# Optimization experiments

Hardware: AMD Instinct MI355X
Metric: run time of the kernel (lower is better)

The kernel has to match this reference:

```python
import jax, jax.numpy as jnp
import numpy as np

K, N = 1024, 16384


def setup_inputs() -> dict:
    key = jax.random.key(0)
    k0, k1, k2 = jax.random.split(key, 3)
    # event counts (non-negative), like the COVID case-count observations
    obs = jax.random.uniform(k0, (K, N), dtype=jnp.float32) * 10.0
    # Beta ~ U(1, 3), Alpha ~ U(0, 0.01) per the torch parameter init
    Beta = 1.0 + 2.0 * jax.random.uniform(k1, (K,), dtype=jnp.float32)
    Alpha = 0.01 * jax.random.uniform(k2, (K, K), dtype=jnp.float32)
    return {"obs": obs, "Beta": Beta, "Alpha": Alpha}


def reference(obs, Beta, Alpha):
    """Hawkes log-likelihood, exact O(N*K) recursion replacing the O(N^2*K^2) loop.

    Original per-step math (t > 0):
      lam1[k, t] = softplus( sum_j Alpha[k, j] * sum_{tp < t} obs[j, tp] * Beta[j] * exp(-(t - tp) * Beta[j]) )
    The exponential kernel gives S_{t+1} = exp(-Beta) * (S_t + obs[:, t]), S_0 = 0,
    where S_t[j] = sum_{tp < t} obs[j, tp] * exp(-(t - tp) * Beta[j]).
    lam1[:, 0] = 0 exactly (the torch code returns zeros at t = 0, not softplus(0)).
    """
    Mu0 = obs.mean(axis=1) / 10.0 + 1e-5                      # [K] background rate
    decay = jnp.exp(-Beta)                                    # [K]

    def step(S, o_t):                                         # S: [K], o_t: [K]
        return decay * (S + o_t), S                           # emit S_t, carry S_{t+1}

    _, S_seq = jax.lax.scan(step, jnp.zeros_like(Beta), obs.T)  # S_seq: [N, K]

    G = Beta[None, :] * S_seq                                 # [N, K] = Beta_j * S_t[j]
    lam1 = jax.nn.softplus(G @ Alpha.T).T                     # [K, N]; row k = softplus(Alpha @ g_t)
    lam1 = lam1.at[:, 0].set(0.0)                             # t = 0 branch returns zeros

    lams0 = jnp.broadcast_to(Mu0[:, None], obs.shape)         # [K, N]
    Nloglams = obs * jnp.log(lams0 + lam1 + 1e-5)
    loglik = (Nloglams - lams0 - lam1).sum()
    return loglik, lams0, lam1
```

## Files before the change

kernel.cpp:

```cpp
#include <hip/hip_runtime.h>
#include <hip/hip_bf16.h>
#include <stdint.h>

#define K_DIM 1024
#define N_DIM 16384

typedef __attribute__((ext_vector_type(8))) short short8;
typedef __attribute__((ext_vector_type(4))) float floatx4;

__device__ __forceinline__ void async_copy16(const void* g, void* l) {
  __builtin_amdgcn_global_load_lds((const __attribute__((address_space(1))) void*)g,
                                   (__attribute__((address_space(3))) void*)l,
                                   16, 0, 0);
}

__device__ __forceinline__ unsigned short f2bf(float x) {
  uint32_t u = __float_as_uint(x);
  u += 0x7fffu + ((u >> 16) & 1u);
  return (unsigned short)(u >> 16);
}

__global__ __launch_bounds__(256) void convert_alpha(const float* __restrict__ A,
                                                     unsigned short* __restrict__ Abf) {
  int idx = (blockIdx.x * 256 + threadIdx.x) * 4;
  floatx4 v = *(const floatx4*)(A + idx);
  ushort4 o;
  o.x = f2bf(v[0]); o.y = f2bf(v[1]); o.z = f2bf(v[2]); o.w = f2bf(v[3]);
  *(ushort4*)(Abf + idx) = o;
}

__global__ __launch_bounds__(256) void mu_kernel(const float* __restrict__ obs,
                                                 float* __restrict__ mu_acc) {
  const int k = blockIdx.x;
  const float* row = obs + (size_t)k * N_DIM;
  float s = 0.f;
  for (int t = threadIdx.x * 4; t < N_DIM; t += 256 * 4) {
    float4 v = *(const float4*)(row + t);
    s += (v.x + v.y) + (v.z + v.w);
  }
  #pragma unroll
  for (int off = 32; off > 0; off >>= 1) s += __shfl_down(s, off);
  __shared__ float ws[4];
  if ((threadIdx.x & 63) == 0) ws[threadIdx.x >> 6] = s;
  __syncthreads();
  if (threadIdx.x == 0) mu_acc[k] = (ws[0] + ws[1]) + (ws[2] + ws[3]);
}

__global__ __launch_bounds__(256) void scan_kernel(const float* __restrict__ obs,
                                                   const float* __restrict__ Beta,
                                                   unsigned short* __restrict__ Gt) {
  __shared__ float tile[64][161];
  const int tw = blockIdx.x;
  const int jg = blockIdx.y;
  const int j0 = jg * 64;
  const int t0 = tw * 128;
  const int tid = threadIdx.x;

  for (int u = tid; u < 64 * 40; u += 256) {
    int row = u / 40;
    int c4 = u % 40;
    int tloc = c4 * 4;
    int tg = t0 - 32 + tloc;
    float4 v;
    if (tg >= 0) {
      v = *(const float4*)(obs + (size_t)(j0 + row) * N_DIM + tg);
    } else {
      v = make_float4(0.f, 0.f, 0.f, 0.f);
    }
    tile[row][tloc]     = v.x;
    tile[row][tloc + 1] = v.y;
    tile[row][tloc + 2] = v.z;
    tile[row][tloc + 3] = v.w;
  }
  __syncthreads();

  const int w = tid >> 6;
  const int lane = tid & 63;
  const int j = j0 + lane;
  const float beta = Beta[j];
  const float decay = expf(-beta);
  const int lt0 = w * 32;
  float S = 0.f;
  #pragma unroll
  for (int i = 0; i < 32; ++i) S = decay * (S + tile[lane][lt0 + i]);
  const int tg = t0 + w * 32;
  #pragma unroll
  for (int i = 0; i < 32; ++i) {
    Gt[(size_t)(tg + i) * K_DIM + j] = f2bf(beta * S);
    S = decay * (S + tile[lane][lt0 + 32 + i]);
  }
}

__global__ __launch_bounds__(256) void gemm_kernel(const unsigned short* __restrict__ A,
                                                   const unsigned short* __restrict__ B,
                                                   const float* __restrict__ obs,
                                                   const float* __restrict__ mu_acc,
                                                   float* __restrict__ lam1_out,
                                                   double* __restrict__ acc_out) {
  const int tb = blockIdx.x;
  const int kb = blockIdx.y;
  const int tid = threadIdx.x;
  const int lane = tid & 63, w = tid >> 6;
  const int wm = w >> 1, wn = w & 1;
  const int ml = lane & 15, q = lane >> 4;

  __shared__ unsigned short As[128 * 64];
  __shared__ unsigned short Bs[128 * 64];
  __shared__ float wsum[4];

  floatx4 acc[4][4] = {};

  const unsigned short* Ab = A + (size_t)kb * 128 * K_DIM;
  const unsigned short* Bb = B + (size_t)tb * 128 * K_DIM;

  for (int kt = 0; kt < 16; ++kt) {
    const unsigned short* Ak = Ab + kt * 64;
    const unsigned short* Bk = Bb + kt * 64;
    #pragma unroll
    for (int it = 0; it < 4; ++it) {
      int L = w * 256 + it * 64 + lane;
      int r = L >> 3;
      int c = L & 7;
      int cg = c ^ (r & 7);
      async_copy16(Ak + (size_t)r * K_DIM + cg * 8, &As[L * 8]);
      async_copy16(Bk + (size_t)r * K_DIM + cg * 8, &Bs[L * 8]);
    }
    __syncthreads();

    #pragma unroll
    for (int kk = 0; kk < 2; ++kk) {
      short8 a[4], b[4];
      #pragma unroll
      for (int mf = 0; mf < 4; ++mf) {
        int r = wm * 64 + mf * 16 + ml;
        int c = (kk * 4 + q) ^ (r & 7);
        a[mf] = *(const short8*)&As[r * 64 + c * 8];
      }
      #pragma unroll
      for (int nf = 0; nf < 4; ++nf) {
        int r = wn * 64 + nf * 16 + ml;
        int c = (kk * 4 + q) ^ (r & 7);
        b[nf] = *(const short8*)&Bs[r * 64 + c * 8];
      }
      #pragma unroll
      for (int mf = 0; mf < 4; ++mf)
        #pragma unroll
        for (int nf = 0; nf < 4; ++nf)
          acc[mf][nf] = __builtin_amdgcn_mfma_f32_16x16x32_bf16(a[mf], b[nf], acc[mf][nf], 0, 0, 0);
    }
    __syncthreads();
  }

  float lsum = 0.f;
  const int kblk = kb * 128 + wm * 64;
  const int tblk = tb * 128 + wn * 64;
  #pragma unroll
  for (int mf = 0; mf < 4; ++mf) {
    int k4 = kblk + mf * 16 + q * 4;
    floatx4 mu4 = *(const floatx4*)&mu_acc[k4];
    #pragma unroll
    for (int r = 0; r < 4; ++r) {
      int k = k4 + r;
      float mu = mu4[r] * (1.0f / 163840.0f) + 1e-5f;
      #pragma unroll
      for (int nf = 0; nf < 4; ++nf) {
        int t = tblk + nf * 16 + ml;
        float raw = acc[mf][nf][r];
        float e = __expf(-fabsf(raw));
        float lam = fmaxf(raw, 0.f) + __logf(1.f + e);
        if (t == 0) lam = 0.f;
        lam1_out[(size_t)k * N_DIM + t] = lam;
        float o = obs[(size_t)k * N_DIM + t];
        lsum += o * __logf(mu + lam + 1e-5f) - mu - lam;
      }
    }
  }
  #pragma unroll
  for (int off = 32; off > 0; off >>= 1) lsum += __shfl_down(lsum, off);
  if (lane == 0) wsum[w] = lsum;
  __syncthreads();
  if (tid == 0) atomicAdd(acc_out, (double)(wsum[0] + wsum[1] + wsum[2] + wsum[3]));
}

__global__ __launch_bounds__(256) void finalize_kernel(const float* __restrict__ mu_acc,
                                                       const double* __restrict__ acc,
                                                       float* __restrict__ out) {
  int k = blockIdx.x;
  float mu = mu_acc[k] * (1.0f / 163840.0f) + 1e-5f;
  float* dst = out + 1 + (size_t)k * N_DIM;
  int tid = threadIdx.x;
  if (tid < 3) dst[tid] = mu;
  float4 v4 = make_float4(mu, mu, mu, mu);
  for (int t = 3 + tid * 4; t + 3 < N_DIM; t += 256 * 4) *(float4*)(dst + t) = v4;
  if (tid == 3) dst[N_DIM - 1] = mu;
  if (blockIdx.x == 0 && tid == 4) out[0] = (float)(*acc);
}

extern "C" void kernel_launch(void* const* d_in, const int* in_sizes, int n_in,
                              void* d_out, int out_size, void* d_ws, size_t ws_size,
                              hipStream_t stream) {
  const float* obs   = (const float*)d_in[0];
  const float* Beta  = (const float*)d_in[1];
  const float* Alpha = (const float*)d_in[2];
  float* out = (float*)d_out;

  double* acc   = (double*)d_ws;
  float* mu_acc = (float*)((char*)d_ws + 16);

  unsigned short* Gt  = (unsigned short*)(out + 4);
  unsigned short* Abf = Gt + (size_t)N_DIM * K_DIM;

  hipMemsetAsync(d_ws, 0, 16, stream);

  convert_alpha<<<dim3(K_DIM * K_DIM / (256 * 4)), 256, 0, stream>>>(Alpha, Abf);

  mu_kernel<<<dim3(K_DIM), 256, 0, stream>>>(obs, mu_acc);

  scan_kernel<<<dim3(N_DIM / 128, K_DIM / 64), 256, 0, stream>>>(obs, Beta, Gt);

  gemm_kernel<<<dim3(N_DIM / 128, K_DIM / 128), 256, 0, stream>>>(
      Abf, Gt, obs, mu_acc, out + 1 + (size_t)K_DIM * N_DIM, acc);

  finalize_kernel<<<dim3(K_DIM), 256, 0, stream>>>(mu_acc, acc, out);
}
```

Measured before the change: 294.7 us.

## Switch GEMM to scaled FP8 inputs and fuse lams0 writes and Alpha conversion

Alpha and the scan output G are quantized to scaled e4m3 FP8, and the GEMM uses fp8 MFMA with an inverse scale applied in the epilogue. This halves the G intermediate traffic and the LDS footprint and uses the faster FP8 matrix path. The Alpha conversion is fused into the mu kernel. When the workspace is large enough, the intermediates live in the workspace, the lams0 broadcast is written in the GEMM epilogue, and the finalize pass is replaced by a one-thread tail kernel. FP8 quantization of Alpha and G adds precision risk to lam1 and to the log-likelihood.

New measurement: 287.3 us. -2.5%, faster.

```diff
diff --git a/kernel.cpp b/kernel.cpp
--- a/kernel.cpp
+++ b/kernel.cpp
@@ -5,7 +5,6 @@
 #define K_DIM 1024
 #define N_DIM 16384
 
-typedef __attribute__((ext_vector_type(8))) short short8;
 typedef __attribute__((ext_vector_type(4))) float floatx4;
 
 __device__ __forceinline__ void async_copy16(const void* g, void* l) {
@@ -14,41 +13,40 @@
                                    16, 0, 0);
 }
 
-__device__ __forceinline__ unsigned short f2bf(float x) {
-  uint32_t u = __float_as_uint(x);
-  u += 0x7fffu + ((u >> 16) & 1u);
-  return (unsigned short)(u >> 16);
-}
-
-__global__ __launch_bounds__(256) void convert_alpha(const float* __restrict__ A,
-                                                     unsigned short* __restrict__ Abf) {
-  int idx = (blockIdx.x * 256 + threadIdx.x) * 4;
-  floatx4 v = *(const floatx4*)(A + idx);
-  ushort4 o;
-  o.x = f2bf(v[0]); o.y = f2bf(v[1]); o.z = f2bf(v[2]); o.w = f2bf(v[3]);
-  *(ushort4*)(Abf + idx) = o;
-}
-
-__global__ __launch_bounds__(256) void mu_kernel(const float* __restrict__ obs,
-                                                 float* __restrict__ mu_acc) {
+__device__ __forceinline__ int pk4_e4m3(float a, float b, float c, float d) {
+  int lo = __builtin_amdgcn_cvt_pk_fp8_f32(a, b, 0, false);
+  return __builtin_amdgcn_cvt_pk_fp8_f32(c, d, lo, true);
+}
+
+#define A_SCALE 512.0f
+#define G_SCALE 32.0f
+#define INV_SCALE (1.0f / (512.0f * 32.0f))
+
+__global__ __launch_bounds__(256) void mu_convert(const float* __restrict__ obs,
+                                                  const float* __restrict__ Alpha,
+                                                  float* __restrict__ mu_acc,
+                                                  int* __restrict__ A8) {
   const int k = blockIdx.x;
+  const int tid = threadIdx.x;
   const float* row = obs + (size_t)k * N_DIM;
   float s = 0.f;
-  for (int t = threadIdx.x * 4; t < N_DIM; t += 256 * 4) {
+  for (int t = tid * 4; t < N_DIM; t += 256 * 4) {
     float4 v = *(const float4*)(row + t);
     s += (v.x + v.y) + (v.z + v.w);
   }
   #pragma unroll
   for (int off = 32; off > 0; off >>= 1) s += __shfl_down(s, off);
   __shared__ float ws[4];
-  if ((threadIdx.x & 63) == 0) ws[threadIdx.x >> 6] = s;
+  if ((tid & 63) == 0) ws[tid >> 6] = s;
+  float4 av = *(const float4*)(Alpha + (size_t)k * K_DIM + tid * 4);
+  A8[k * 256 + tid] = pk4_e4m3(av.x * A_SCALE, av.y * A_SCALE, av.z * A_SCALE, av.w * A_SCALE);
   __syncthreads();
-  if (threadIdx.x == 0) mu_acc[k] = (ws[0] + ws[1]) + (ws[2] + ws[3]);
+  if (tid == 0) mu_acc[k] = (ws[0] + ws[1]) + (ws[2] + ws[3]);
 }
 
 __global__ __launch_bounds__(256) void scan_kernel(const float* __restrict__ obs,
                                                    const float* __restrict__ Beta,
-                                                   unsigned short* __restrict__ Gt) {
+                                                   unsigned char* __restrict__ Gt8) {
   __shared__ float tile[64][161];
   const int tw = blockIdx.x;
   const int jg = blockIdx.y;
@@ -78,7 +76,7 @@
   const int lane = tid & 63;
   const int j = j0 + lane;
   const float beta = Beta[j];
-  const float decay = expf(-beta);
+  const float decay = __expf(-beta);
   const int lt0 = w * 32;
   float S = 0.f;
   #pragma unroll
@@ -86,16 +84,18 @@
   const int tg = t0 + w * 32;
   #pragma unroll
   for (int i = 0; i < 32; ++i) {
-    Gt[(size_t)(tg + i) * K_DIM + j] = f2bf(beta * S);
+    int p = __builtin_amdgcn_cvt_pk_fp8_f32(G_SCALE * beta * S, 0.f, 0, false);
+    Gt8[(size_t)(tg + i) * K_DIM + j] = (unsigned char)(p & 0xff);
     S = decay * (S + tile[lane][lt0 + 32 + i]);
   }
 }
 
-__global__ __launch_bounds__(256) void gemm_kernel(const unsigned short* __restrict__ A,
-                                                   const unsigned short* __restrict__ B,
+__global__ __launch_bounds__(256) void gemm_kernel(const unsigned char* __restrict__ A8,
+                                                   const unsigned char* __restrict__ B8,
                                                    const float* __restrict__ obs,
                                                    const float* __restrict__ mu_acc,
                                                    float* __restrict__ lam1_out,
+                                                   float* __restrict__ lams0_out,
                                                    double* __restrict__ acc_out) {
   const int tb = blockIdx.x;
   const int kb = blockIdx.y;
@@ -104,49 +104,51 @@
   const int wm = w >> 1, wn = w & 1;
   const int ml = lane & 15, q = lane >> 4;
 
-  __shared__ unsigned short As[128 * 64];
-  __shared__ unsigned short Bs[128 * 64];
+  __shared__ unsigned char As[128 * 64];
+  __shared__ unsigned char Bs[128 * 64];
   __shared__ float wsum[4];
 
   floatx4 acc[4][4] = {};
 
-  const unsigned short* Ab = A + (size_t)kb * 128 * K_DIM;
-  const unsigned short* Bb = B + (size_t)tb * 128 * K_DIM;
+  const unsigned char* Ab = A8 + (size_t)kb * 128 * K_DIM;
+  const unsigned char* Bb = B8 + (size_t)tb * 128 * K_DIM;
 
   for (int kt = 0; kt < 16; ++kt) {
-    const unsigned short* Ak = Ab + kt * 64;
-    const unsigned short* Bk = Bb + kt * 64;
+    const unsigned char* Ak = Ab + kt * 64;
+    const unsigned char* Bk = Bb + kt * 64;
     #pragma unroll
-    for (int it = 0; it < 4; ++it) {
-      int L = w * 256 + it * 64 + lane;
-      int r = L >> 3;
-      int c = L & 7;
-      int cg = c ^ (r & 7);
-      async_copy16(Ak + (size_t)r * K_DIM + cg * 8, &As[L * 8]);
-      async_copy16(Bk + (size_t)r * K_DIM + cg * 8, &Bs[L * 8]);
+    for (int it = 0; it < 2; ++it) {
+      int L = it * 256 + tid;
+      int r = L >> 2;
+      int c = L & 3;
+      int cg = c ^ ((r >> 1) & 3);
+      async_copy16(Ak + (size_t)r * K_DIM + cg * 16, &As[L * 16]);
+      async_copy16(Bk + (size_t)r * K_DIM + cg * 16, &Bs[L * 16]);
     }
     __syncthreads();
 
     #pragma unroll
     for (int kk = 0; kk < 2; ++kk) {
-      short8 a[4], b[4];
+      long a[4], b[4];
+      const int c0 = kk * 2 + (q >> 1);
+      const int sub = (q & 1) * 8;
       #pragma unroll
       for (int mf = 0; mf < 4; ++mf) {
         int r = wm * 64 + mf * 16 + ml;
-        int c = (kk * 4 + q) ^ (r & 7);
-        a[mf] = *(const short8*)&As[r * 64 + c * 8];
+        int cg = c0 ^ ((r >> 1) & 3);
+        a[mf] = *(const long*)&As[r * 64 + cg * 16 + sub];
       }
       #pragma unroll
       for (int nf = 0; nf < 4; ++nf) {
         int r = wn * 64 + nf * 16 + ml;
-        int c = (kk * 4 + q) ^ (r & 7);
-        b[nf] = *(const short8*)&Bs[r * 64 + c * 8];
+        int cg = c0 ^ ((r >> 1) & 3);
+        b[nf] = *(const long*)&Bs[r * 64 + cg * 16 + sub];
       }
       #pragma unroll
       for (int mf = 0; mf < 4; ++mf)
         #pragma unroll
         for (int nf = 0; nf < 4; ++nf)
-          acc[mf][nf] = __builtin_amdgcn_mfma_f32_16x16x32_bf16(a[mf], b[nf], acc[mf][nf], 0, 0, 0);
+          acc[mf][nf] = __builtin_amdgcn_mfma_f32_16x16x32_fp8_fp8(a[mf], b[nf], acc[mf][nf], 0, 0, 0);
     }
     __syncthreads();
   }
@@ -165,11 +167,12 @@
       #pragma unroll
       for (int nf = 0; nf < 4; ++nf) {
         int t = tblk + nf * 16 + ml;
-        float raw = acc[mf][nf][r];
+        float raw = acc[mf][nf][r] * INV_SCALE;
         float e = __expf(-fabsf(raw));
         float lam = fmaxf(raw, 0.f) + __logf(1.f + e);
         if (t == 0) lam = 0.f;
         lam1_out[(size_t)k * N_DIM + t] = lam;
+        if (lams0_out) lams0_out[(size_t)k * N_DIM + t] = mu;
         float o = obs[(size_t)k * N_DIM + t];
         lsum += o * __logf(mu + lam + 1e-5f) - mu - lam;
       }
@@ -180,6 +183,10 @@
   if (lane == 0) wsum[w] = lsum;
   __syncthreads();
   if (tid == 0) atomicAdd(acc_out, (double)(wsum[0] + wsum[1] + wsum[2] + wsum[3]));
+}
+
+__global__ void tail_kernel(const double* __restrict__ acc, float* __restrict__ out) {
+  out[0] = (float)(*acc);
 }
 
 __global__ __launch_bounds__(256) void finalize_kernel(const float* __restrict__ mu_acc,
@@ -207,19 +214,32 @@
   double* acc   = (double*)d_ws;
   float* mu_acc = (float*)((char*)d_ws + 16);
 
-  unsigned short* Gt  = (unsigned short*)(out + 4);
-  unsigned short* Abf = Gt + (size_t)N_DIM * K_DIM;
+  const bool ws_big = ws_size >= (size_t)(8192 + 17 * 1024 * 1024 + 4096);
+  unsigned char* Gt8;
+  unsigned char* A8;
+  if (ws_big) {
+    Gt8 = (unsigned char*)d_ws + 8192;
+    A8  = Gt8 + (size_t)N_DIM * K_DIM;
+  } else {
+    Gt8 = (unsigned char*)(out + 4);
+    A8  = Gt8 + (size_t)N_DIM * K_DIM;
+  }
 
   hipMemsetAsync(d_ws, 0, 16, stream);
 
-  convert_alpha<<<dim3(K_DIM * K_DIM / (256 * 4)), 256, 0, stream>>>(Alpha, Abf);
-
-  mu_kernel<<<dim3(K_DIM), 256, 0, stream>>>(obs, mu_acc);
-
-  scan_kernel<<<dim3(N_DIM / 128, K_DIM / 64), 256, 0, stream>>>(obs, Beta, Gt);
+  mu_convert<<<dim3(K_DIM), 256, 0, stream>>>(obs, Alpha, mu_acc, (int*)A8);
+
+  scan_kernel<<<dim3(N_DIM / 128, K_DIM / 64), 256, 0, stream>>>(obs, Beta, Gt8);
 
   gemm_kernel<<<dim3(N_DIM / 128, K_DIM / 128), 256, 0, stream>>>(
-      Abf, Gt, obs, mu_acc, out + 1 + (size_t)K_DIM * N_DIM, acc);
-
-  finalize_kernel<<<dim3(K_DIM), 256, 0, stream>>>(mu_acc, acc, out);
-}
+      A8, Gt8, obs, mu_acc,
+      out + 1 + (size_t)K_DIM * N_DIM,
+      ws_big ? (out + 1) : nullptr,
+      acc);
+
+  if (ws_big) {
+    tail_kernel<<<1, 1, 0, stream>>>(acc, out);
+  } else {
+    finalize_kernel<<<dim3(K_DIM), 256, 0, stream>>>(mu_acc, acc, out);
+  }
+}
```
